# Optimization experiments

Measured on AMD Instinct MI355X. Metric: run time of the kernel, lower is better.

## Reference

```python
import jax, jax.numpy as jnp
import numpy as np

B, S, E, H = 4, 8192, 1024, 16
D = E // H  # head_dim = 64


def setup_inputs() -> dict:
    key = jax.random.key(0)
    ks = jax.random.split(key, 9)
    s = 0.02
    return {
        "x": jax.random.normal(ks[0], (B, S, E), dtype=jnp.float32),
        "Wq": jax.random.normal(ks[1], (D, E), dtype=jnp.float32) * s,
        "bq": jax.random.normal(ks[2], (D,), dtype=jnp.float32) * s,
        "Wk": jax.random.normal(ks[3], (D, E), dtype=jnp.float32) * s,
        "bk": jax.random.normal(ks[4], (D,), dtype=jnp.float32) * s,
        "Wv": jax.random.normal(ks[5], (D, E), dtype=jnp.float32) * s,
        "bv": jax.random.normal(ks[6], (D,), dtype=jnp.float32) * s,
        "Wo": jax.random.normal(ks[7], (E, E), dtype=jnp.float32) * s,
        "bo": jax.random.normal(ks[8], (E,), dtype=jnp.float32) * s,
    }


def reference(x, Wq, bq, Wk, bk, Wv, bv, Wo, bo):
    b, s, e = x.shape
    d = Wq.shape[0]          # head_dim (projections map embed_dim -> head_dim)
    h = e // d               # num_heads
    # torch Linear: y = x @ W.T + b ; projected shape [B, S, d]
    # view(B, -1, h, d) on [B, S, d] => effective seq S' = S // h (faithful to source)
    def split_heads(t):
        return t.reshape(b, -1, h, d).transpose(0, 2, 1, 3)  # [B, H, S', D]
    q = split_heads(x @ Wq.T + bq)
    k = split_heads(x @ Wk.T + bk)
    v = split_heads(x @ Wv.T + bv)
    scores = jnp.einsum('bhqd,bhkd->bhqk', q, k) / np.sqrt(d).astype(jnp.float32)
    attn = jax.nn.softmax(scores, axis=-1)  # dropout=0.0 => identity
    ctx = jnp.einsum('bhqk,bhkd->bhqd', attn, v)
    ctx = ctx.transpose(0, 2, 1, 3).reshape(b, -1, e)  # [B, S', E]
    return ctx @ Wo.T + bo
```

## Files before the change

### kernel.cpp

```cpp
#include <hip/hip_runtime.h>
#include <hip/hip_bf16.h>


typedef unsigned short u16;
typedef __attribute__((ext_vector_type(8))) short short8;
typedef __attribute__((ext_vector_type(4))) float f32x4;

__device__ inline u16 f2bf(float f) {
    union { float f; unsigned u; } v; v.f = f;
    unsigned u = v.u;
    return (u16)((u + 0x7fffu + ((u >> 16) & 1u)) >> 16);
}
__device__ inline unsigned pack_bf2(float a, float b) {
    union { __hip_bfloat162 h; unsigned u; } v;
    v.h = __float22bfloat162_rn(float2{a, b});
    return v.u;
}

__global__ __launch_bounds__(256) void convw(
    const float* __restrict__ Wq, const float* __restrict__ bq,
    const float* __restrict__ Wk, const float* __restrict__ bk,
    const float* __restrict__ Wv, const float* __restrict__ bv,
    const float* __restrict__ Wo,
    u16* __restrict__ Wqkv, float* __restrict__ qkvb, u16* __restrict__ Wob)
{
    const int idx = blockIdx.x * 256 + threadIdx.x;
    Wob[idx] = f2bf(Wo[idx]);
    if (idx < 196608) {
        const int row = idx >> 10, k = idx & 1023;
        float v = (row < 64)  ? Wq[row * 1024 + k] * 0.125f
                : (row < 128) ? Wk[(row - 64) * 1024 + k]
                              : Wv[(row - 128) * 1024 + k];
        Wqkv[idx] = f2bf(v);
    }
    if (idx < 192) {
        qkvb[idx] = (idx < 64) ? bq[idx] * 0.125f
                  : (idx < 128) ? bk[idx - 64] : bv[idx - 128];
    }
}

__global__ __launch_bounds__(256) void qkv_gemm(
    const float* __restrict__ X, const u16* __restrict__ W,
    const float* __restrict__ bias, u16* __restrict__ Out)
{
    __shared__ short8 As[4 * 64];
    __shared__ short8 Bs[12 * 64];

    const int tid = threadIdx.x;
    const int lane = tid & 63, wid = tid >> 6;
    const long m0 = (long)blockIdx.x * 64;

    const int ra = tid >> 2;
    const int ka = tid & 3;
    const int aslot = (ra >> 4) * 64 + ka * 16 + (ra & 15);
    const float* px = X + (m0 + ra) * 1024 + ka * 8;

    f32x4 acc[12] = {};

    for (int k0 = 0; k0 < 1024; k0 += 32) {
        float4 x0 = *(const float4*)(px + k0);
        float4 x1 = *(const float4*)(px + k0 + 4);
        union { short8 s; unsigned u[4]; } av;
        av.u[0] = pack_bf2(x0.x, x0.y);
        av.u[1] = pack_bf2(x0.z, x0.w);
        av.u[2] = pack_bf2(x1.x, x1.y);
        av.u[3] = pack_bf2(x1.z, x1.w);
        short8 bv[3];
        #pragma unroll
        for (int i = 0; i < 3; ++i) {
            const int c = tid + 256 * i;
            bv[i] = *(const short8*)(W + (long)(c >> 2) * 1024 + k0 + (c & 3) * 8);
        }
        __syncthreads();
        As[aslot] = av.s;
        #pragma unroll
        for (int i = 0; i < 3; ++i) {
            const int c = tid + 256 * i, rb = c >> 2;
            Bs[(rb >> 4) * 64 + (c & 3) * 16 + (rb & 15)] = bv[i];
        }
        __syncthreads();
        short8 af = As[wid * 64 + lane];
        #pragma unroll
        for (int nt = 0; nt < 12; ++nt)
            acc[nt] = __builtin_amdgcn_mfma_f32_16x16x32_bf16(
                af, Bs[nt * 64 + lane], acc[nt], 0, 0, 0);
    }

    const int q = lane >> 4, r = lane & 15;
    #pragma unroll
    for (int nt = 0; nt < 12; ++nt) {
        const int col = nt * 16 + r;
        const float badd = bias[col];
        #pragma unroll
        for (int e = 0; e < 4; ++e) {
            const long row = m0 + wid * 16 + q * 4 + e;
            Out[row * 192 + col] = f2bf(acc[nt][e] + badd);
        }
    }
}

__global__ __launch_bounds__(256) void vtrans(
    const u16* __restrict__ qkv, u16* __restrict__ Vt)
{
    __shared__ u16 T[64][68];
    const int bh = blockIdx.x, b = bh >> 4, h = bh & 15;
    const int i0 = blockIdx.y * 64;
    const int tid = threadIdx.x;

    #pragma unroll
    for (int it = 0; it < 2; ++it) {
        const int c = tid + 256 * it;
        const int il = c >> 3, d8 = (c & 7) * 8;
        short8 v = *(const short8*)(qkv +
            ((long)b * 8192 + (long)(i0 + il) * 16 + h) * 192 + 128 + d8);
        #pragma unroll
        for (int j = 0; j < 8; ++j) T[d8 + j][il] = (u16)v[j];
    }
    __syncthreads();
    #pragma unroll
    for (int it = 0; it < 2; ++it) {
        const int c = tid + 256 * it;
        const int dl = c >> 3, i8 = (c & 7) * 8;
        short8 o;
        #pragma unroll
        for (int j = 0; j < 8; ++j) o[j] = (short)T[dl][i8 + j];
        *(short8*)(Vt + ((long)bh * 64 + dl) * 512 + i0 + i8) = o;
    }
}

__global__ __launch_bounds__(256) void attn_flash(
    const u16* __restrict__ qkv, const u16* __restrict__ Vt,
    u16* __restrict__ ctx)
{
    __shared__ u16 Plds[4][16 * 72];

    const int tid = threadIdx.x, lane = tid & 63, wid = tid >> 6;
    const int q = lane >> 4, r = lane & 15;
    const int qt = blockIdx.x;
    const int bh = blockIdx.y;
    const int b = bh >> 4, h = bh & 15;

    const long qrowbase = (long)b * 8192 + h;

    short8 Qf0, Qf1;
    {
        const int i = qt * 64 + wid * 16 + r;
        const u16* p = qkv + (qrowbase + (long)i * 16) * 192 + q * 8;
        Qf0 = *(const short8*)(p);
        Qf1 = *(const short8*)(p + 32);
    }

    f32x4 O[4] = {};
    float mrun[4] = {-1e30f, -1e30f, -1e30f, -1e30f};
    float lrun[4] = {};
    u16* Pw = &Plds[wid][0];

    for (int j0 = 0; j0 < 512; j0 += 64) {
        f32x4 S[4];
        #pragma unroll
        for (int ct = 0; ct < 4; ++ct) {
            const int key = j0 + ct * 16 + r;
            const u16* p = qkv + (qrowbase + (long)key * 16) * 192 + 64 + q * 8;
            short8 k0 = *(const short8*)(p);
            short8 k1 = *(const short8*)(p + 32);
            f32x4 s = {};
            s = __builtin_amdgcn_mfma_f32_16x16x32_bf16(Qf0, k0, s, 0, 0, 0);
            s = __builtin_amdgcn_mfma_f32_16x16x32_bf16(Qf1, k1, s, 0, 0, 0);
            S[ct] = s;
        }
        #pragma unroll
        for (int e = 0; e < 4; ++e) {
            float mc = fmaxf(fmaxf(S[0][e], S[1][e]), fmaxf(S[2][e], S[3][e]));
            #pragma unroll
            for (int off = 1; off < 16; off <<= 1)
                mc = fmaxf(mc, __shfl_xor(mc, off, 64));
            const float mnew = fmaxf(mrun[e], mc);
            const float alpha = __expf(mrun[e] - mnew);
            mrun[e] = mnew;
            float se = 0.f;
            #pragma unroll
            for (int ct = 0; ct < 4; ++ct) {
                const float pv = __expf(S[ct][e] - mnew);
                S[ct][e] = pv; se += pv;
            }
            #pragma unroll
            for (int off = 1; off < 16; off <<= 1)
                se += __shfl_xor(se, off, 64);
            lrun[e] = lrun[e] * alpha + se;
            #pragma unroll
            for (int nt = 0; nt < 4; ++nt) O[nt][e] *= alpha;
        }
        #pragma unroll
        for (int e = 0; e < 4; ++e)
            #pragma unroll
            for (int ct = 0; ct < 4; ++ct)
                Pw[(q * 4 + e) * 72 + ct * 16 + r] = f2bf(S[ct][e]);
        short8 Pf0 = *(const short8*)(Pw + r * 72 + q * 8);
        short8 Pf1 = *(const short8*)(Pw + r * 72 + 32 + q * 8);
        #pragma unroll
        for (int nt = 0; nt < 4; ++nt) {
            const u16* p = Vt + ((long)bh * 64 + nt * 16 + r) * 512 + j0 + q * 8;
            short8 v0 = *(const short8*)(p);
            short8 v1 = *(const short8*)(p + 32);
            O[nt] = __builtin_amdgcn_mfma_f32_16x16x32_bf16(Pf0, v0, O[nt], 0, 0, 0);
            O[nt] = __builtin_amdgcn_mfma_f32_16x16x32_bf16(Pf1, v1, O[nt], 0, 0, 0);
        }
    }

    #pragma unroll
    for (int e = 0; e < 4; ++e) {
        const float inv = 1.0f / lrun[e];
        const long i = qt * 64 + wid * 16 + q * 4 + e;
        u16* po = ctx + ((long)b * 512 + i) * 1024 + h * 64 + r;
        #pragma unroll
        for (int nt = 0; nt < 4; ++nt)
            po[nt * 16] = f2bf(O[nt][e] * inv);
    }
}

__global__ __launch_bounds__(256) void gemm_bf(
    const u16* __restrict__ A, long lda,
    const u16* __restrict__ B, long ldb,
    const float* __restrict__ bias,
    float* __restrict__ C, long ldc, int K)
{
    __shared__ short8 As[4 * 64];
    __shared__ short8 Bs[4 * 64];

    const int tid = threadIdx.x;
    const int lane = tid & 63, wid = tid >> 6;
    const long m0 = (long)blockIdx.x * 64, n0 = (long)blockIdx.y * 64;

    const int r4 = tid >> 2, k8 = tid & 3;
    const int slot = (r4 >> 4) * 64 + k8 * 16 + (r4 & 15);
    const u16* pa = A + (m0 + r4) * lda + k8 * 8;
    const u16* pb = B + (n0 + r4) * ldb + k8 * 8;

    const int mh = (wid >> 1) * 2, nh = (wid & 1) * 2;
    f32x4 acc[2][2] = {};

    for (int k0 = 0; k0 < K; k0 += 32) {
        short8 av = *(const short8*)(pa + k0);
        short8 bv = *(const short8*)(pb + k0);
        __syncthreads();
        As[slot] = av; Bs[slot] = bv;
        __syncthreads();
        short8 af0 = As[(mh + 0) * 64 + lane], af1 = As[(mh + 1) * 64 + lane];
        short8 bf0 = Bs[(nh + 0) * 64 + lane], bf1 = Bs[(nh + 1) * 64 + lane];
        acc[0][0] = __builtin_amdgcn_mfma_f32_16x16x32_bf16(af0, bf0, acc[0][0], 0, 0, 0);
        acc[0][1] = __builtin_amdgcn_mfma_f32_16x16x32_bf16(af0, bf1, acc[0][1], 0, 0, 0);
        acc[1][0] = __builtin_amdgcn_mfma_f32_16x16x32_bf16(af1, bf0, acc[1][0], 0, 0, 0);
        acc[1][1] = __builtin_amdgcn_mfma_f32_16x16x32_bf16(af1, bf1, acc[1][1], 0, 0, 0);
    }

    const int q = lane >> 4, r = lane & 15;
    #pragma unroll
    for (int i = 0; i < 2; ++i)
        #pragma unroll
        for (int j = 0; j < 2; ++j) {
            const long col = n0 + (nh + j) * 16 + r;
            const float badd = bias[col];
            #pragma unroll
            for (int e = 0; e < 4; ++e) {
                const long row = m0 + (mh + i) * 16 + q * 4 + e;
                C[row * ldc + col] = acc[i][j][e] + badd;
            }
        }
}

extern "C" void kernel_launch(void* const* d_in, const int* in_sizes, int n_in,
                              void* d_out, int out_size, void* d_ws, size_t ws_size,
                              hipStream_t stream)
{
    const float* x  = (const float*)d_in[0];
    const float* Wq = (const float*)d_in[1];
    const float* bq = (const float*)d_in[2];
    const float* Wk = (const float*)d_in[3];
    const float* bk = (const float*)d_in[4];
    const float* Wv = (const float*)d_in[5];
    const float* bv = (const float*)d_in[6];
    const float* Wo = (const float*)d_in[7];
    const float* bo = (const float*)d_in[8];
    float* out = (float*)d_out;
    char* ws = (char*)d_ws;

    u16*   qkv  = (u16*)(ws);
    u16*   Vt   = (u16*)(ws + 12582912);
    u16*   Wqkv = (u16*)(ws + 16777216);
    u16*   Wob  = (u16*)(ws + 17170432);
    float* qkvb = (float*)(ws + 19267584);
    u16*   ctx  = (u16*)(ws + 19268352);

    convw<<<4096, 256, 0, stream>>>(Wq, bq, Wk, bk, Wv, bv, Wo, Wqkv, qkvb, Wob);
    qkv_gemm<<<512, 256, 0, stream>>>(x, Wqkv, qkvb, qkv);
    vtrans<<<dim3(64, 8), 256, 0, stream>>>(qkv, Vt);
    attn_flash<<<dim3(8, 64), 256, 0, stream>>>(qkv, Vt, ctx);
    gemm_bf<<<dim3(32, 16), 256, 0, stream>>>(
        ctx, 1024, Wob, 1024, bo, out, 1024, 1024);
}
```

Measured before the change: 285.0 us.

## Double-buffer GEMM and attention operands via direct global-to-LDS loads

Replaces register-staged LDS fills with global_load_lds async copies into double-buffered shared memory in the QKV GEMM, the flash attention kernel and the output GEMM. The next tile is fetched while the current one is consumed, and one barrier per iteration replaces two. The QKV GEMM now reads X directly into per-wave MFMA fragments, skipping LDS for A, and the output GEMM uses a K step of 64. In exchange it uses more LDS, which can lower occupancy, and relies on the barrier ordering the async LDS writes correctly.

New measurement: 273.8 us. -3.9%, faster.

```diff
diff --git a/kernel.cpp b/kernel.cpp
--- a/kernel.cpp
+++ b/kernel.cpp
@@ -15,6 +15,12 @@
     union { __hip_bfloat162 h; unsigned u; } v;
     v.h = __float22bfloat162_rn(float2{a, b});
     return v.u;
+}
+__device__ __forceinline__ void gld16(void* lds, const void* gptr) {
+    __builtin_amdgcn_global_load_lds(
+        (const __attribute__((address_space(1))) unsigned int*)gptr,
+        (__attribute__((address_space(3))) unsigned int*)lds,
+        16, 0, 0);
 }
 
 __global__ __launch_bounds__(256) void convw(
@@ -43,50 +49,52 @@
     const float* __restrict__ X, const u16* __restrict__ W,
     const float* __restrict__ bias, u16* __restrict__ Out)
 {
-    __shared__ short8 As[4 * 64];
-    __shared__ short8 Bs[12 * 64];
+    __shared__ short8 Bs[2][768];
 
     const int tid = threadIdx.x;
     const int lane = tid & 63, wid = tid >> 6;
+    const int q = lane >> 4, r = lane & 15;
     const long m0 = (long)blockIdx.x * 64;
 
-    const int ra = tid >> 2;
-    const int ka = tid & 3;
-    const int aslot = (ra >> 4) * 64 + ka * 16 + (ra & 15);
-    const float* px = X + (m0 + ra) * 1024 + ka * 8;
+    const u16* wp[3];
+    #pragma unroll
+    for (int i = 0; i < 3; ++i)
+        wp[i] = W + (long)((wid * 3 + i) * 16 + r) * 1024 + q * 8;
+
+    const float* px = X + (m0 + wid * 16 + r) * 1024 + q * 8;
 
     f32x4 acc[12] = {};
 
+    #pragma unroll
+    for (int i = 0; i < 3; ++i)
+        gld16(&Bs[0][wid * 192 + i * 64], wp[i]);
+    float4 a0 = *(const float4*)(px);
+    float4 a1 = *(const float4*)(px + 4);
+    __syncthreads();
+
     for (int k0 = 0; k0 < 1024; k0 += 32) {
-        float4 x0 = *(const float4*)(px + k0);
-        float4 x1 = *(const float4*)(px + k0 + 4);
-        union { short8 s; unsigned u[4]; } av;
-        av.u[0] = pack_bf2(x0.x, x0.y);
-        av.u[1] = pack_bf2(x0.z, x0.w);
-        av.u[2] = pack_bf2(x1.x, x1.y);
-        av.u[3] = pack_bf2(x1.z, x1.w);
-        short8 bv[3];
-        #pragma unroll
-        for (int i = 0; i < 3; ++i) {
-            const int c = tid + 256 * i;
-            bv[i] = *(const short8*)(W + (long)(c >> 2) * 1024 + k0 + (c & 3) * 8);
-        }
-        __syncthreads();
-        As[aslot] = av.s;
-        #pragma unroll
-        for (int i = 0; i < 3; ++i) {
-            const int c = tid + 256 * i, rb = c >> 2;
-            Bs[(rb >> 4) * 64 + (c & 3) * 16 + (rb & 15)] = bv[i];
-        }
-        __syncthreads();
-        short8 af = As[wid * 64 + lane];
+        const int buf = (k0 >> 5) & 1;
+        float4 a0n = {}, a1n = {};
+        if (k0 + 32 < 1024) {
+            #pragma unroll
+            for (int i = 0; i < 3; ++i)
+                gld16(&Bs[buf ^ 1][wid * 192 + i * 64], wp[i] + k0 + 32);
+            a0n = *(const float4*)(px + k0 + 32);
+            a1n = *(const float4*)(px + k0 + 36);
+        }
+        union { short8 s; unsigned u[4]; } af;
+        af.u[0] = pack_bf2(a0.x, a0.y);
+        af.u[1] = pack_bf2(a0.z, a0.w);
+        af.u[2] = pack_bf2(a1.x, a1.y);
+        af.u[3] = pack_bf2(a1.z, a1.w);
         #pragma unroll
         for (int nt = 0; nt < 12; ++nt)
             acc[nt] = __builtin_amdgcn_mfma_f32_16x16x32_bf16(
-                af, Bs[nt * 64 + lane], acc[nt], 0, 0, 0);
-    }
-
-    const int q = lane >> 4, r = lane & 15;
+                af.s, Bs[buf][nt * 64 + lane], acc[nt], 0, 0, 0);
+        __syncthreads();
+        a0 = a0n; a1 = a1n;
+    }
+
     #pragma unroll
     for (int nt = 0; nt < 12; ++nt) {
         const int col = nt * 16 + r;
@@ -132,6 +140,8 @@
     const u16* __restrict__ qkv, const u16* __restrict__ Vt,
     u16* __restrict__ ctx)
 {
+    __shared__ short8 Ks[2][512];
+    __shared__ short8 Vs[2][512];
     __shared__ u16 Plds[4][16 * 72];
 
     const int tid = threadIdx.x, lane = tid & 63, wid = tid >> 6;
@@ -139,7 +149,6 @@
     const int qt = blockIdx.x;
     const int bh = blockIdx.y;
     const int b = bh >> 4, h = bh & 15;
-
     const long qrowbase = (long)b * 8192 + h;
 
     short8 Qf0, Qf1;
@@ -150,22 +159,39 @@
         Qf1 = *(const short8*)(p + 32);
     }
 
+    const u16* kbase = qkv + (qrowbase + (long)(wid * 16 + r) * 16) * 192
+                           + 64 + q * 8;
+    const u16* vbase = Vt + ((long)bh * 64 + wid * 16 + r) * 512 + q * 8;
+
+    gld16(&Ks[0][wid * 64],       kbase);
+    gld16(&Ks[0][256 + wid * 64], kbase + 32);
+    gld16(&Vs[0][wid * 64],       vbase);
+    gld16(&Vs[0][256 + wid * 64], vbase + 32);
+    __syncthreads();
+
     f32x4 O[4] = {};
     float mrun[4] = {-1e30f, -1e30f, -1e30f, -1e30f};
     float lrun[4] = {};
     u16* Pw = &Plds[wid][0];
 
-    for (int j0 = 0; j0 < 512; j0 += 64) {
+    for (int c = 0; c < 8; ++c) {
+        const int j0 = c * 64, buf = c & 1;
+        if (c < 7) {
+            const u16* kp = kbase + (long)(j0 + 64) * 3072;
+            const u16* vp = vbase + j0 + 64;
+            gld16(&Ks[buf ^ 1][wid * 64],       kp);
+            gld16(&Ks[buf ^ 1][256 + wid * 64], kp + 32);
+            gld16(&Vs[buf ^ 1][wid * 64],       vp);
+            gld16(&Vs[buf ^ 1][256 + wid * 64], vp + 32);
+        }
         f32x4 S[4];
         #pragma unroll
         for (int ct = 0; ct < 4; ++ct) {
-            const int key = j0 + ct * 16 + r;
-            const u16* p = qkv + (qrowbase + (long)key * 16) * 192 + 64 + q * 8;
-            short8 k0 = *(const short8*)(p);
-            short8 k1 = *(const short8*)(p + 32);
             f32x4 s = {};
-            s = __builtin_amdgcn_mfma_f32_16x16x32_bf16(Qf0, k0, s, 0, 0, 0);
-            s = __builtin_amdgcn_mfma_f32_16x16x32_bf16(Qf1, k1, s, 0, 0, 0);
+            s = __builtin_amdgcn_mfma_f32_16x16x32_bf16(
+                Qf0, Ks[buf][ct * 64 + lane], s, 0, 0, 0);
+            s = __builtin_amdgcn_mfma_f32_16x16x32_bf16(
+                Qf1, Ks[buf][256 + ct * 64 + lane], s, 0, 0, 0);
             S[ct] = s;
         }
         #pragma unroll
@@ -199,12 +225,12 @@
         short8 Pf1 = *(const short8*)(Pw + r * 72 + 32 + q * 8);
         #pragma unroll
         for (int nt = 0; nt < 4; ++nt) {
-            const u16* p = Vt + ((long)bh * 64 + nt * 16 + r) * 512 + j0 + q * 8;
-            short8 v0 = *(const short8*)(p);
-            short8 v1 = *(const short8*)(p + 32);
-            O[nt] = __builtin_amdgcn_mfma_f32_16x16x32_bf16(Pf0, v0, O[nt], 0, 0, 0);
-            O[nt] = __builtin_amdgcn_mfma_f32_16x16x32_bf16(Pf1, v1, O[nt], 0, 0, 0);
-        }
+            O[nt] = __builtin_amdgcn_mfma_f32_16x16x32_bf16(
+                Pf0, Vs[buf][nt * 64 + lane], O[nt], 0, 0, 0);
+            O[nt] = __builtin_amdgcn_mfma_f32_16x16x32_bf16(
+                Pf1, Vs[buf][256 + nt * 64 + lane], O[nt], 0, 0, 0);
+        }
+        __syncthreads();
     }
 
     #pragma unroll
@@ -218,52 +244,70 @@
     }
 }
 
-__global__ __launch_bounds__(256) void gemm_bf(
-    const u16* __restrict__ A, long lda,
-    const u16* __restrict__ B, long ldb,
-    const float* __restrict__ bias,
-    float* __restrict__ C, long ldc, int K)
-{
-    __shared__ short8 As[4 * 64];
-    __shared__ short8 Bs[4 * 64];
+__global__ __launch_bounds__(256) void gemm_o(
+    const u16* __restrict__ A, const u16* __restrict__ B,
+    const float* __restrict__ bias, float* __restrict__ C)
+{
+    __shared__ short8 As[2][512];
+    __shared__ short8 Bs[2][512];
 
     const int tid = threadIdx.x;
     const int lane = tid & 63, wid = tid >> 6;
+    const int q = lane >> 4, r = lane & 15;
     const long m0 = (long)blockIdx.x * 64, n0 = (long)blockIdx.y * 64;
-
-    const int r4 = tid >> 2, k8 = tid & 3;
-    const int slot = (r4 >> 4) * 64 + k8 * 16 + (r4 & 15);
-    const u16* pa = A + (m0 + r4) * lda + k8 * 8;
-    const u16* pb = B + (n0 + r4) * ldb + k8 * 8;
-
-    const int mh = (wid >> 1) * 2, nh = (wid & 1) * 2;
+    const int wm = wid >> 1, wn = wid & 1;
+
+    const u16* ap[2];
+    const u16* bp[2];
+    #pragma unroll
+    for (int i = 0; i < 2; ++i) {
+        const int t = wid * 2 + i, f = t >> 2, mt = t & 3;
+        ap[i] = A + (m0 + mt * 16 + r) * 1024 + f * 32 + q * 8;
+        bp[i] = B + (n0 + mt * 16 + r) * 1024 + f * 32 + q * 8;
+    }
+
+    #pragma unroll
+    for (int i = 0; i < 2; ++i) {
+        gld16(&As[0][(wid * 2 + i) * 64], ap[i]);
+        gld16(&Bs[0][(wid * 2 + i) * 64], bp[i]);
+    }
+    __syncthreads();
+
     f32x4 acc[2][2] = {};
 
-    for (int k0 = 0; k0 < K; k0 += 32) {
-        short8 av = *(const short8*)(pa + k0);
-        short8 bv = *(const short8*)(pb + k0);
+    for (int k0 = 0; k0 < 1024; k0 += 64) {
+        const int buf = (k0 >> 6) & 1;
+        if (k0 + 64 < 1024) {
+            #pragma unroll
+            for (int i = 0; i < 2; ++i) {
+                gld16(&As[buf ^ 1][(wid * 2 + i) * 64], ap[i] + k0 + 64);
+                gld16(&Bs[buf ^ 1][(wid * 2 + i) * 64], bp[i] + k0 + 64);
+            }
+        }
+        #pragma unroll
+        for (int f = 0; f < 2; ++f) {
+            short8 af0 = As[buf][f * 256 + (wm * 2 + 0) * 64 + lane];
+            short8 af1 = As[buf][f * 256 + (wm * 2 + 1) * 64 + lane];
+            short8 bf0 = Bs[buf][f * 256 + (wn * 2 + 0) * 64 + lane];
+            short8 bf1 = Bs[buf][f * 256 + (wn * 2 + 1) * 64 + lane];
+            acc[0][0] = __builtin_amdgcn_mfma_f32_16x16x32_bf16(af0, bf0, acc[0][0], 0, 0, 0);
+            acc[0][1] = __builtin_amdgcn_mfma_f32_16x16x32_bf16(af0, bf1, acc[0][1], 0, 0, 0);
+            acc[1][0] = __builtin_amdgcn_mfma_f32_16x16x32_bf16(af1, bf0, acc[1][0], 0, 0, 0);
+            acc[1][1] = __builtin_amdgcn_mfma_f32_16x16x32_bf16(af1, bf1, acc[1][1], 0, 0, 0);
+        }
         __syncthreads();
-        As[slot] = av; Bs[slot] = bv;
-        __syncthreads();
-        short8 af0 = As[(mh + 0) * 64 + lane], af1 = As[(mh + 1) * 64 + lane];
-        short8 bf0 = Bs[(nh + 0) * 64 + lane], bf1 = Bs[(nh + 1) * 64 + lane];
-        acc[0][0] = __builtin_amdgcn_mfma_f32_16x16x32_bf16(af0, bf0, acc[0][0], 0, 0, 0);
-        acc[0][1] = __builtin_amdgcn_mfma_f32_16x16x32_bf16(af0, bf1, acc[0][1], 0, 0, 0);
-        acc[1][0] = __builtin_amdgcn_mfma_f32_16x16x32_bf16(af1, bf0, acc[1][0], 0, 0, 0);
-        acc[1][1] = __builtin_amdgcn_mfma_f32_16x16x32_bf16(af1, bf1, acc[1][1], 0, 0, 0);
-    }
-
-    const int q = lane >> 4, r = lane & 15;
+    }
+
     #pragma unroll
     for (int i = 0; i < 2; ++i)
         #pragma unroll
         for (int j = 0; j < 2; ++j) {
-            const long col = n0 + (nh + j) * 16 + r;
+            const long col = n0 + (wn * 2 + j) * 16 + r;
             const float badd = bias[col];
             #pragma unroll
             for (int e = 0; e < 4; ++e) {
-                const long row = m0 + (mh + i) * 16 + q * 4 + e;
-                C[row * ldc + col] = acc[i][j][e] + badd;
+                const long row = m0 + (wm * 2 + i) * 16 + q * 4 + e;
+                C[row * 1024 + col] = acc[i][j][e] + badd;
             }
         }
 }
@@ -295,6 +339,5 @@
     qkv_gemm<<<512, 256, 0, stream>>>(x, Wqkv, qkvb, qkv);
     vtrans<<<dim3(64, 8), 256, 0, stream>>>(qkv, Vt);
     attn_flash<<<dim3(8, 64), 256, 0, stream>>>(qkv, Vt, ctx);
-    gemm_bf<<<dim3(32, 16), 256, 0, stream>>>(
-        ctx, 1024, Wob, 1024, bo, out, 1024, 1024);
-}
+    gemm_o<<<dim3(32, 16), 256, 0, stream>>>(ctx, Wob, bo, out);
+}
```

## Drop LDS staging in GEMMs and repack K contiguously for attention

Applied to the files above, without the earlier changes.

The QKV and output GEMMs now load MFMA fragments straight from global memory into registers, removing the shared-memory staging and both barriers per k-step, with an unroll of 2 and an occupancy hint in the launch bounds. The V-transpose kernel also writes a contiguous per-head K copy so attention reads K with unit stride instead of gathering rows strided by 192 elements. This trades barrier and LDS traffic for redundant global/L2 reads: each wave re-fetches weight fragments the block used to share, and the extra K copy adds write traffic.

After: 348.3 us. 22.2% more time.

```diff
diff --git a/kernel.cpp b/kernel.cpp
--- a/kernel.cpp
+++ b/kernel.cpp
@@ -39,54 +39,37 @@
     }
 }
 
-__global__ __launch_bounds__(256) void qkv_gemm(
+__global__ __launch_bounds__(256, 2) void qkv_gemm(
     const float* __restrict__ X, const u16* __restrict__ W,
     const float* __restrict__ bias, u16* __restrict__ Out)
 {
-    __shared__ short8 As[4 * 64];
-    __shared__ short8 Bs[12 * 64];
-
     const int tid = threadIdx.x;
     const int lane = tid & 63, wid = tid >> 6;
+    const int q = lane >> 4, r = lane & 15;
     const long m0 = (long)blockIdx.x * 64;
 
-    const int ra = tid >> 2;
-    const int ka = tid & 3;
-    const int aslot = (ra >> 4) * 64 + ka * 16 + (ra & 15);
-    const float* px = X + (m0 + ra) * 1024 + ka * 8;
+    const float* px = X + (m0 + wid * 16 + r) * 1024 + q * 8;
+    const u16*   pb = W + (long)r * 1024 + q * 8;
 
     f32x4 acc[12] = {};
 
+    #pragma unroll 2
     for (int k0 = 0; k0 < 1024; k0 += 32) {
-        float4 x0 = *(const float4*)(px + k0);
-        float4 x1 = *(const float4*)(px + k0 + 4);
-        union { short8 s; unsigned u[4]; } av;
-        av.u[0] = pack_bf2(x0.x, x0.y);
-        av.u[1] = pack_bf2(x0.z, x0.w);
-        av.u[2] = pack_bf2(x1.x, x1.y);
-        av.u[3] = pack_bf2(x1.z, x1.w);
-        short8 bv[3];
-        #pragma unroll
-        for (int i = 0; i < 3; ++i) {
-            const int c = tid + 256 * i;
-            bv[i] = *(const short8*)(W + (long)(c >> 2) * 1024 + k0 + (c & 3) * 8);
-        }
-        __syncthreads();
-        As[aslot] = av.s;
-        #pragma unroll
-        for (int i = 0; i < 3; ++i) {
-            const int c = tid + 256 * i, rb = c >> 2;
-            Bs[(rb >> 4) * 64 + (c & 3) * 16 + (rb & 15)] = bv[i];
-        }
-        __syncthreads();
-        short8 af = As[wid * 64 + lane];
-        #pragma unroll
-        for (int nt = 0; nt < 12; ++nt)
+        float4 a0 = *(const float4*)(px + k0);
+        float4 a1 = *(const float4*)(px + k0 + 4);
+        union { short8 s; unsigned u[4]; } af;
+        af.u[0] = pack_bf2(a0.x, a0.y);
+        af.u[1] = pack_bf2(a0.z, a0.w);
+        af.u[2] = pack_bf2(a1.x, a1.y);
+        af.u[3] = pack_bf2(a1.z, a1.w);
+        #pragma unroll
+        for (int nt = 0; nt < 12; ++nt) {
+            short8 bf = *(const short8*)(pb + nt * 16384 + k0);
             acc[nt] = __builtin_amdgcn_mfma_f32_16x16x32_bf16(
-                af, Bs[nt * 64 + lane], acc[nt], 0, 0, 0);
-    }
-
-    const int q = lane >> 4, r = lane & 15;
+                af.s, bf, acc[nt], 0, 0, 0);
+        }
+    }
+
     #pragma unroll
     for (int nt = 0; nt < 12; ++nt) {
         const int col = nt * 16 + r;
@@ -99,8 +82,8 @@
     }
 }
 
-__global__ __launch_bounds__(256) void vtrans(
-    const u16* __restrict__ qkv, u16* __restrict__ Vt)
+__global__ __launch_bounds__(256) void kvtrans(
+    const u16* __restrict__ qkv, u16* __restrict__ Kc, u16* __restrict__ Vt)
 {
     __shared__ u16 T[64][68];
     const int bh = blockIdx.x, b = bh >> 4, h = bh & 15;
@@ -111,10 +94,12 @@
     for (int it = 0; it < 2; ++it) {
         const int c = tid + 256 * it;
         const int il = c >> 3, d8 = (c & 7) * 8;
-        short8 v = *(const short8*)(qkv +
-            ((long)b * 8192 + (long)(i0 + il) * 16 + h) * 192 + 128 + d8);
-        #pragma unroll
-        for (int j = 0; j < 8; ++j) T[d8 + j][il] = (u16)v[j];
+        const u16* src = qkv + ((long)b * 8192 + (long)(i0 + il) * 16 + h) * 192;
+        short8 kv = *(const short8*)(src + 64 + d8);
+        *(short8*)(Kc + ((long)bh * 512 + i0 + il) * 64 + d8) = kv;
+        short8 vv = *(const short8*)(src + 128 + d8);
+        #pragma unroll
+        for (int j = 0; j < 8; ++j) T[d8 + j][il] = (u16)vv[j];
     }
     __syncthreads();
     #pragma unroll
@@ -128,9 +113,9 @@
     }
 }
 
-__global__ __launch_bounds__(256) void attn_flash(
-    const u16* __restrict__ qkv, const u16* __restrict__ Vt,
-    u16* __restrict__ ctx)
+__global__ __launch_bounds__(256, 2) void attn_flash(
+    const u16* __restrict__ qkv, const u16* __restrict__ Kc,
+    const u16* __restrict__ Vt, u16* __restrict__ ctx)
 {
     __shared__ u16 Plds[4][16 * 72];
 
@@ -139,7 +124,6 @@
     const int qt = blockIdx.x;
     const int bh = blockIdx.y;
     const int b = bh >> 4, h = bh & 15;
-
     const long qrowbase = (long)b * 8192 + h;
 
     short8 Qf0, Qf1;
@@ -150,6 +134,9 @@
         Qf1 = *(const short8*)(p + 32);
     }
 
+    const u16* kb = Kc + ((long)bh * 512 + r) * 64 + q * 8;
+    const u16* vb = Vt + ((long)bh * 64 + r) * 512 + q * 8;
+
     f32x4 O[4] = {};
     float mrun[4] = {-1e30f, -1e30f, -1e30f, -1e30f};
     float lrun[4] = {};
@@ -159,8 +146,7 @@
         f32x4 S[4];
         #pragma unroll
         for (int ct = 0; ct < 4; ++ct) {
-            const int key = j0 + ct * 16 + r;
-            const u16* p = qkv + (qrowbase + (long)key * 16) * 192 + 64 + q * 8;
+            const u16* p = kb + (long)(j0 + ct * 16) * 64;
             short8 k0 = *(const short8*)(p);
             short8 k1 = *(const short8*)(p + 32);
             f32x4 s = {};
@@ -199,7 +185,7 @@
         short8 Pf1 = *(const short8*)(Pw + r * 72 + 32 + q * 8);
         #pragma unroll
         for (int nt = 0; nt < 4; ++nt) {
-            const u16* p = Vt + ((long)bh * 64 + nt * 16 + r) * 512 + j0 + q * 8;
+            const u16* p = vb + (long)nt * 16 * 512 + j0;
             short8 v0 = *(const short8*)(p);
             short8 v1 = *(const short8*)(p + 32);
             O[nt] = __builtin_amdgcn_mfma_f32_16x16x32_bf16(Pf0, v0, O[nt], 0, 0, 0);
@@ -218,52 +204,45 @@
     }
 }
 
-__global__ __launch_bounds__(256) void gemm_bf(
-    const u16* __restrict__ A, long lda,
-    const u16* __restrict__ B, long ldb,
-    const float* __restrict__ bias,
-    float* __restrict__ C, long ldc, int K)
-{
-    __shared__ short8 As[4 * 64];
-    __shared__ short8 Bs[4 * 64];
-
+__global__ __launch_bounds__(256, 2) void gemm_o(
+    const u16* __restrict__ A, const u16* __restrict__ B,
+    const float* __restrict__ bias, float* __restrict__ C)
+{
     const int tid = threadIdx.x;
     const int lane = tid & 63, wid = tid >> 6;
+    const int q = lane >> 4, r = lane & 15;
     const long m0 = (long)blockIdx.x * 64, n0 = (long)blockIdx.y * 64;
-
-    const int r4 = tid >> 2, k8 = tid & 3;
-    const int slot = (r4 >> 4) * 64 + k8 * 16 + (r4 & 15);
-    const u16* pa = A + (m0 + r4) * lda + k8 * 8;
-    const u16* pb = B + (n0 + r4) * ldb + k8 * 8;
-
-    const int mh = (wid >> 1) * 2, nh = (wid & 1) * 2;
+    const int wm = wid >> 1, wn = wid & 1;
+
+    const u16* pa0 = A + (m0 + (wm * 2 + 0) * 16 + r) * 1024 + q * 8;
+    const u16* pa1 = A + (m0 + (wm * 2 + 1) * 16 + r) * 1024 + q * 8;
+    const u16* pb0 = B + (n0 + (wn * 2 + 0) * 16 + r) * 1024 + q * 8;
+    const u16* pb1 = B + (n0 + (wn * 2 + 1) * 16 + r) * 1024 + q * 8;
+
     f32x4 acc[2][2] = {};
 
-    for (int k0 = 0; k0 < K; k0 += 32) {
-        short8 av = *(const short8*)(pa + k0);
-        short8 bv = *(const short8*)(pb + k0);
-        __syncthreads();
-        As[slot] = av; Bs[slot] = bv;
-        __syncthreads();
-        short8 af0 = As[(mh + 0) * 64 + lane], af1 = As[(mh + 1) * 64 + lane];
-        short8 bf0 = Bs[(nh + 0) * 64 + lane], bf1 = Bs[(nh + 1) * 64 + lane];
+    #pragma unroll 2
+    for (int k0 = 0; k0 < 1024; k0 += 32) {
+        short8 af0 = *(const short8*)(pa0 + k0);
+        short8 af1 = *(const short8*)(pa1 + k0);
+        short8 bf0 = *(const short8*)(pb0 + k0);
+        short8 bf1 = *(const short8*)(pb1 + k0);
         acc[0][0] = __builtin_amdgcn_mfma_f32_16x16x32_bf16(af0, bf0, acc[0][0], 0, 0, 0);
         acc[0][1] = __builtin_amdgcn_mfma_f32_16x16x32_bf16(af0, bf1, acc[0][1], 0, 0, 0);
         acc[1][0] = __builtin_amdgcn_mfma_f32_16x16x32_bf16(af1, bf0, acc[1][0], 0, 0, 0);
         acc[1][1] = __builtin_amdgcn_mfma_f32_16x16x32_bf16(af1, bf1, acc[1][1], 0, 0, 0);
     }
 
-    const int q = lane >> 4, r = lane & 15;
     #pragma unroll
     for (int i = 0; i < 2; ++i)
         #pragma unroll
         for (int j = 0; j < 2; ++j) {
-            const long col = n0 + (nh + j) * 16 + r;
+            const long col = n0 + (wn * 2 + j) * 16 + r;
             const float badd = bias[col];
             #pragma unroll
             for (int e = 0; e < 4; ++e) {
-                const long row = m0 + (mh + i) * 16 + q * 4 + e;
-                C[row * ldc + col] = acc[i][j][e] + badd;
+                const long row = m0 + (wm * 2 + i) * 16 + q * 4 + e;
+                C[row * 1024 + col] = acc[i][j][e] + badd;
             }
         }
 }
@@ -286,15 +265,15 @@
 
     u16*   qkv  = (u16*)(ws);
     u16*   Vt   = (u16*)(ws + 12582912);
-    u16*   Wqkv = (u16*)(ws + 16777216);
-    u16*   Wob  = (u16*)(ws + 17170432);
-    float* qkvb = (float*)(ws + 19267584);
-    u16*   ctx  = (u16*)(ws + 19268352);
+    u16*   Kc   = (u16*)(ws + 16777216);
+    u16*   Wqkv = (u16*)(ws + 20971520);
+    u16*   Wob  = (u16*)(ws + 21364736);
+    float* qkvb = (float*)(ws + 23461888);
+    u16*   ctx  = (u16*)(ws + 23462656);
 
     convw<<<4096, 256, 0, stream>>>(Wq, bq, Wk, bk, Wv, bv, Wo, Wqkv, qkvb, Wob);
     qkv_gemm<<<512, 256, 0, stream>>>(x, Wqkv, qkvb, qkv);
-    vtrans<<<dim3(64, 8), 256, 0, stream>>>(qkv, Vt);
-    attn_flash<<<dim3(8, 64), 256, 0, stream>>>(qkv, Vt, ctx);
-    gemm_bf<<<dim3(32, 16), 256, 0, stream>>>(
-        ctx, 1024, Wob, 1024, bo, out, 1024, 1024);
-}
+    kvtrans<<<dim3(64, 8), 256, 0, stream>>>(qkv, Kc, Vt);
+    attn_flash<<<dim3(8, 64), 256, 0, stream>>>(qkv, Kc, Vt, ctx);
+    gemm_o<<<dim3(32, 16), 256, 0, stream>>>(ctx, Wob, bo, out);
+}
```
